# Performance work log

Hardware: AMD Instinct MI355X
Metric: run time of the kernel (lower is better)

The kernel has to match this reference:

```python
import jax, jax.numpy as jnp
import numpy as np

L, B, N, C, H = 6, 4, 512, 512, 8
D = C // H          # head_dim = 64
MLP = 4 * C         # mlp_ratio = 4.0
EPS = 1e-6


def setup_inputs() -> dict:
    key = jax.random.key(0)
    ks = jax.random.split(key, 12)
    p = lambda k, sh: jax.random.normal(k, sh, dtype=jnp.float32) * 0.02
    return {
        "x": jax.random.normal(ks[0], (B, N, C), dtype=jnp.float32),
        "time_emb": jax.random.normal(ks[1], (B, C), dtype=jnp.float32),
        "pair_emb": jax.random.normal(ks[2], (B, H, N, N), dtype=jnp.float32) * 0.1,
        "is_padded_mask": jnp.zeros((B, 1, 1, N), dtype=bool),
        # per-block stacked params (leading dim = L blocks)
        "wq": p(ks[3], (L, C, C)),
        "wk": p(ks[4], (L, C, C)),
        "wv": p(ks[5], (L, C, C)),
        "wo": p(ks[6], (L, C, C)),
        "bo": jnp.zeros((L, C), dtype=jnp.float32),
        "w1": p(ks[7], (L, C, MLP)),
        "b1": jnp.zeros((L, MLP), dtype=jnp.float32),
        "w2": p(ks[8], (L, MLP, C)),
        "b2": jnp.zeros((L, C), dtype=jnp.float32),
        "wada": p(ks[9], (L, C, 6 * C)),
        "bada": jnp.zeros((L, 6 * C), dtype=jnp.float32),
    }


def _ln(x):
    # LayerNorm without affine, eps=1e-6 (torch elementwise_affine=False)
    mu = jnp.mean(x, axis=-1, keepdims=True)
    var = jnp.mean(jnp.square(x - mu), axis=-1, keepdims=True)
    return (x - mu) * jax.lax.rsqrt(var + EPS)


def _modulate(x, shift, scale):
    return x * (1.0 + scale[:, None, :]) + shift[:, None, :]


def reference(x, time_emb, pair_emb, is_padded_mask,
              wq, wk, wv, wo, bo, w1, b1, w2, b2, wada, bada):
    scale = D ** -0.5
    t_act = jax.nn.silu(time_emb)  # shared SiLU input to adaLN of each block
    for i in range(L):
        ada = t_act @ wada[i] + bada[i]  # (B, 6C)
        sh_msa, sc_msa, g_msa, sh_mlp, sc_mlp, g_mlp = jnp.split(ada, 6, axis=1)
        # fill_attn_mask: masked_fill padded key positions with -inf
        pair = jnp.where(is_padded_mask, -jnp.inf, pair_emb)  # (B,H,N,N)
        mx = _modulate(_ln(x), sh_msa, sc_msa)  # (B,N,C)
        q = (mx @ wq[i]).reshape(B, N, H, D)
        k = (mx @ wk[i]).reshape(B, N, H, D)
        v = (mx @ wv[i]).reshape(B, N, H, D)
        qk = jnp.einsum('bnhd,bshd->bhns', q, k) * scale  # (B,H,N,N)
        attn = jax.nn.softmax(qk + pair, axis=-1)
        o = jnp.einsum('bhns,bshd->bnhd', attn, v).reshape(B, N, C)
        o = o @ wo[i] + bo[i]
        x = x + g_msa[:, None, :] * o
        pair_emb = pair + qk  # residual on pair embedding
        h = _modulate(_ln(x), sh_mlp, sc_mlp)
        h = jax.nn.gelu(h @ w1[i] + b1[i], approximate=True) @ w2[i] + b2[i]
        x = x + g_mlp[:, None, :] * h
    return x, pair_emb
```

## Files before the change

kernel.cpp:

```cpp
#include <hip/hip_runtime.h>
#include <hip/hip_bf16.h>

#define LNUM 6
#define BB 4
#define NSEQ 512
#define CDIM 512
#define HNUM 8
#define DHEAD 64
#define MLPD 2048
#define MROWS (BB*NSEQ)

typedef __hip_bfloat16 bf16;
typedef __attribute__((ext_vector_type(4))) float f32x4;
typedef __attribute__((ext_vector_type(8))) short bf16x8;

__device__ __forceinline__ void gld_lds16(const bf16* g, bf16* l) {
  __builtin_amdgcn_global_load_lds((const __attribute__((address_space(1))) void*)g,
                                   (__attribute__((address_space(3))) void*)l, 16, 0, 0);
}

__device__ __forceinline__ short f2bs(float f) {
  bf16 h = __float2bfloat16(f);
  short s; __builtin_memcpy(&s, &h, 2); return s;
}

__device__ __forceinline__ float gelu_tanh(float t) {
  float u = 0.7978845608028654f * (t + 0.044715f * t * t * t);
  u = fminf(fmaxf(u, -15.f), 15.f);
  float e = __expf(2.f * u);
  return 0.5f * t * (1.f + (e - 1.f) / (e + 1.f));
}

enum { EP_BF16 = 0, EP_RESID = 2, EP_GELU = 3 };

template<int MODE>
__global__ __launch_bounds__(256) void gemm_nt(
    const bf16* __restrict__ A, int lda,
    const bf16* __restrict__ Bt, int ldb,
    int K, int zdiv,
    long sA1, long sA2, long sB1, long sB2, long sO1, long sO2,
    bf16* __restrict__ obf, int ldo,
    const float* __restrict__ bias,
    const float* __restrict__ ada, int gate_off,
    float* __restrict__ xres)
{
  __shared__ bf16 lA[2 * 64 * 64];
  __shared__ bf16 lB[2 * 64 * 64];
  const int tid = threadIdx.x;
  const int wid = tid >> 6, lane = tid & 63;
  const int z = blockIdx.z;
  const long z1 = z / zdiv, z2 = z % zdiv;
  A  += z1 * sA1 + z2 * sA2;
  Bt += z1 * sB1 + z2 * sB2;
  const long obase = z1 * sO1 + z2 * sO2;
  const int m0 = blockIdx.x * 64;
  const int n0 = blockIdx.y * 64;
  const int wm = wid >> 1, wn = wid & 1;
  const int srow = tid >> 3, scl = tid & 7;

  f32x4 zero = {0.f, 0.f, 0.f, 0.f};
  f32x4 acc[2][2];
#pragma unroll
  for (int i = 0; i < 2; i++)
#pragma unroll
    for (int j = 0; j < 2; j++) acc[i][j] = zero;

  auto stage = [&](int buf, int kt) {
#pragma unroll
    for (int r = 0; r < 2; r++) {
      const int rr = (r << 5) + srow;
      const int gk = (scl ^ (rr & 7)) << 3;
      gld_lds16(A + (size_t)(m0 + rr) * lda + (kt << 6) + gk,
                lA + buf * 4096 + (r << 11) + (wid << 9));
    }
#pragma unroll
    for (int r = 0; r < 2; r++) {
      const int rr = (r << 5) + srow;
      const int gk = (scl ^ (rr & 7)) << 3;
      gld_lds16(Bt + (size_t)(n0 + rr) * ldb + (kt << 6) + gk,
                lB + buf * 4096 + (r << 11) + (wid << 9));
    }
  };

  const int rlo = lane & 15, kq = lane >> 4;
  auto compute = [&](int buf) {
    bf16x8 af[2][2], bg[2][2];
#pragma unroll
    for (int kk = 0; kk < 2; kk++) {
#pragma unroll
      for (int i = 0; i < 2; i++) {
        const int ra = (wm << 5) + (i << 4) + rlo;
        af[kk][i] = *(const bf16x8*)(lA + buf * 4096 + (ra << 6) +
                                     ((((kk << 2) + kq) ^ (ra & 7)) << 3));
        const int rb2 = (wn << 5) + (i << 4) + rlo;
        bg[kk][i] = *(const bf16x8*)(lB + buf * 4096 + (rb2 << 6) +
                                     ((((kk << 2) + kq) ^ (rb2 & 7)) << 3));
      }
    }
#pragma unroll
    for (int kk = 0; kk < 2; kk++)
#pragma unroll
      for (int i = 0; i < 2; i++)
#pragma unroll
        for (int j = 0; j < 2; j++)
          acc[i][j] = __builtin_amdgcn_mfma_f32_16x16x32_bf16(af[kk][i], bg[kk][j], acc[i][j], 0, 0, 0);
  };

  const int NT = K >> 6;
  stage(0, 0);
  for (int t = 0; t < NT - 1; t++) {
    stage((t + 1) & 1, t + 1);
    asm volatile("s_waitcnt vmcnt(4)" ::: "memory");
    __builtin_amdgcn_s_barrier();
    asm volatile("" ::: "memory");
    compute(t & 1);
    asm volatile("" ::: "memory");
    __builtin_amdgcn_s_barrier();
  }
  asm volatile("s_waitcnt vmcnt(0)" ::: "memory");
  __builtin_amdgcn_s_barrier();
  asm volatile("" ::: "memory");
  compute((NT - 1) & 1);

  const int cl = lane & 15, rb = (lane >> 4) << 2;
#pragma unroll
  for (int i = 0; i < 2; i++) {
#pragma unroll
    for (int j = 0; j < 2; j++) {
      const int gc = n0 + (wn << 5) + (j << 4) + cl;
#pragma unroll
      for (int r = 0; r < 4; r++) {
        const int gr = m0 + (wm << 5) + (i << 4) + rb + r;
        float v = acc[i][j][r];
        if (MODE == EP_BF16) {
          obf[obase + (size_t)gr * ldo + gc] = __float2bfloat16(v);
        } else if (MODE == EP_RESID) {
          const int b = gr >> 9;
          float t2 = v + bias[gc];
          xres[(size_t)gr * CDIM + gc] += ada[b * (6 * CDIM) + gate_off + gc] * t2;
        } else {
          float t2 = v + bias[gc];
          obf[obase + (size_t)gr * ldo + gc] = __float2bfloat16(gelu_tanh(t2));
        }
      }
    }
  }
}

__global__ __launch_bounds__(256) void attn_fused(
    const bf16* __restrict__ qkv, const bf16* __restrict__ vt,
    const float* __restrict__ pair_in, float* __restrict__ pair_out,
    const unsigned char* __restrict__ mask,
    bf16* __restrict__ obuf, float scale)
{
  __shared__ bf16 lQ[64 * 64];
  __shared__ bf16 lK[2][64 * 64];
  __shared__ bf16 lV[2][64 * 64];
  __shared__ bf16 lP[64 * 64];
  const int tid = threadIdx.x, wid = tid >> 6, lane = tid & 63;
  const int z = blockIdx.z, b = z >> 3, h = z & 7;
  const int m0 = blockIdx.x * 64;
  const int srow = tid >> 3, scl = tid & 7;
  const bf16* Aq = qkv + (size_t)b * NSEQ * 1536 + h * 64;
  const bf16* Bk = Aq + CDIM;
  const bf16* Bv = vt + (size_t)z * DHEAD * NSEQ;
  const size_t pz = (size_t)z * NSEQ * NSEQ;

#pragma unroll
  for (int r = 0; r < 2; r++) {
    const int rr = (r << 5) + srow;
    const int gk = (scl ^ (rr & 7)) << 3;
    gld_lds16(Aq + (size_t)(m0 + rr) * 1536 + gk, lQ + (r << 11) + (wid << 9));
    gld_lds16(Bk + (size_t)rr * 1536 + gk, lK[0] + (r << 11) + (wid << 9));
    gld_lds16(Bv + (size_t)rr * NSEQ + gk, lV[0] + (r << 11) + (wid << 9));
  }

  const int rlo = lane & 15, kq = lane >> 4, cl = rlo;
  float m_run[4], l_run[4];
  f32x4 oacc[4];
  f32x4 zero = {0.f, 0.f, 0.f, 0.f};
#pragma unroll
  for (int r = 0; r < 4; r++) { m_run[r] = -INFINITY; l_run[r] = 0.f; }
#pragma unroll
  for (int j = 0; j < 4; j++) oacc[j] = zero;
  bf16x8 afq[2];

  for (int ct = 0; ct < 8; ct++) {
    const int cur = ct & 1;
    asm volatile("s_waitcnt vmcnt(0)" ::: "memory");
    __builtin_amdgcn_s_barrier();
    asm volatile("" ::: "memory");

    if (ct < 7) {
#pragma unroll
      for (int r = 0; r < 2; r++) {
        const int rr = (r << 5) + srow;
        const int gk = (scl ^ (rr & 7)) << 3;
        gld_lds16(Bk + (size_t)((ct + 1) * 64 + rr) * 1536 + gk,
                  lK[cur ^ 1] + (r << 11) + (wid << 9));
        gld_lds16(Bv + (size_t)rr * NSEQ + (ct + 1) * 64 + gk,
                  lV[cur ^ 1] + (r << 11) + (wid << 9));
      }
    }

    if (ct == 0) {
#pragma unroll
      for (int kk = 0; kk < 2; kk++) {
        const int ra = (wid << 4) + rlo;
        afq[kk] = *(const bf16x8*)(lQ + (ra << 6) + ((((kk << 1) << 1) + kq) == 0 ? 0 : 0));
      }
#pragma unroll
      for (int kk = 0; kk < 2; kk++) {
        const int ra = (wid << 4) + rlo;
        afq[kk] = *(const bf16x8*)(lQ + (ra << 6) + ((((kk << 2) + kq) ^ (ra & 7)) << 3));
      }
    }

    float pr[4][4];
#pragma unroll
    for (int j = 0; j < 4; j++)
#pragma unroll
      for (int r = 0; r < 4; r++)
        pr[j][r] = pair_in[pz + (size_t)(m0 + (wid << 4) + (kq << 2) + r) * NSEQ +
                           (ct * 64 + (j << 4) + cl)];
    bool mk[4];
#pragma unroll
    for (int j = 0; j < 4; j++)
      mk[j] = mask[b * NSEQ + ct * 64 + (j << 4) + cl] != 0;

    f32x4 s[4];
#pragma unroll
    for (int j = 0; j < 4; j++) s[j] = zero;
#pragma unroll
    for (int kk = 0; kk < 2; kk++)
#pragma unroll
      for (int j = 0; j < 4; j++) {
        const int rk = (j << 4) + rlo;
        bf16x8 bk = *(const bf16x8*)(lK[cur] + (rk << 6) + ((((kk << 2) + kq) ^ (rk & 7)) << 3));
        s[j] = __builtin_amdgcn_mfma_f32_16x16x32_bf16(afq[kk], bk, s[j], 0, 0, 0);
      }

    float p[4][4];
#pragma unroll
    for (int r = 0; r < 4; r++) {
      const size_t prow = pz + (size_t)(m0 + (wid << 4) + (kq << 2) + r) * NSEQ + ct * 64;
      float sf[4];
#pragma unroll
      for (int j = 0; j < 4; j++) {
        float pp = mk[j] ? -INFINITY : pr[j][r];
        sf[j] = s[j][r] * scale + pp;
        pair_out[prow + (j << 4) + cl] = sf[j];
      }
      float tm = fmaxf(fmaxf(sf[0], sf[1]), fmaxf(sf[2], sf[3]));
#pragma unroll
      for (int o = 1; o < 16; o <<= 1) tm = fmaxf(tm, __shfl_xor(tm, o));
      const float mnew = fmaxf(m_run[r], tm);
      const float fr = __expf(m_run[r] - mnew);
      float rs = 0.f;
#pragma unroll
      for (int j = 0; j < 4; j++) { p[j][r] = __expf(sf[j] - mnew); rs += p[j][r]; }
#pragma unroll
      for (int o = 1; o < 16; o <<= 1) rs += __shfl_xor(rs, o);
      l_run[r] = l_run[r] * fr + rs;
      m_run[r] = mnew;
#pragma unroll
      for (int j = 0; j < 4; j++) oacc[j][r] *= fr;
    }

#pragma unroll
    for (int j = 0; j < 4; j++)
#pragma unroll
      for (int r = 0; r < 4; r++) {
        const int row = (wid << 4) + (kq << 2) + r;
        const int col = (j << 4) + cl;
        lP[(row << 6) + (((col >> 3) ^ (row & 7)) << 3) + (col & 7)] = __float2bfloat16(p[j][r]);
      }
    asm volatile("s_waitcnt lgkmcnt(0)" ::: "memory");
    __builtin_amdgcn_sched_barrier(0);

#pragma unroll
    for (int kk = 0; kk < 2; kk++) {
      const int ra = (wid << 4) + rlo;
      bf16x8 ap = *(const bf16x8*)(lP + (ra << 6) + ((((kk << 2) + kq) ^ (ra & 7)) << 3));
#pragma unroll
      for (int j = 0; j < 4; j++) {
        const int rd = (j << 4) + rlo;
        bf16x8 bv = *(const bf16x8*)(lV[cur] + (rd << 6) + ((((kk << 2) + kq) ^ (rd & 7)) << 3));
        oacc[j] = __builtin_amdgcn_mfma_f32_16x16x32_bf16(ap, bv, oacc[j], 0, 0, 0);
      }
    }
  }

#pragma unroll
  for (int j = 0; j < 4; j++)
#pragma unroll
    for (int r = 0; r < 4; r++) {
      const int gr = m0 + (wid << 4) + (kq << 2) + r;
      const int gc = h * 64 + (j << 4) + cl;
      obuf[((size_t)b * NSEQ + gr) * CDIM + gc] = __float2bfloat16(oacc[j][r] / l_run[r]);
    }
}

__global__ __launch_bounds__(256) void ln_mod(const float* __restrict__ x,
                                              const float* __restrict__ ada,
                                              int sh_off, int sc_off,
                                              bf16* __restrict__ out)
{
  const int row = blockIdx.x;
  const int b = row >> 9;
  const float* xr = x + (size_t)row * CDIM;
  const int t = threadIdx.x;
  float2 v = ((const float2*)xr)[t];
  float s = v.x + v.y;
  float ss = v.x * v.x + v.y * v.y;
#pragma unroll
  for (int o = 32; o > 0; o >>= 1) { s += __shfl_down(s, o); ss += __shfl_down(ss, o); }
  __shared__ float red[8];
  __shared__ float mv[2];
  const int w = t >> 6, ln = t & 63;
  if (ln == 0) { red[w] = s; red[4 + w] = ss; }
  __syncthreads();
  if (t == 0) {
    float S = red[0] + red[1] + red[2] + red[3];
    float SS = red[4] + red[5] + red[6] + red[7];
    float mu = S * (1.0f / CDIM);
    float var = SS * (1.0f / CDIM) - mu * mu;
    mv[0] = mu; mv[1] = rsqrtf(var + 1e-6f);
  }
  __syncthreads();
  const float mu = mv[0], rs = mv[1];
  const float* adab = ada + b * (6 * CDIM);
  const int c = t * 2;
  float o0 = (v.x - mu) * rs * (1.0f + adab[sc_off + c])     + adab[sh_off + c];
  float o1 = (v.y - mu) * rs * (1.0f + adab[sc_off + c + 1]) + adab[sh_off + c + 1];
  out[(size_t)row * CDIM + c]     = __float2bfloat16(o0);
  out[(size_t)row * CDIM + c + 1] = __float2bfloat16(o1);
}

__global__ __launch_bounds__(256) void ada_part(const float* __restrict__ te,
                                                const float* __restrict__ wada,
                                                float* __restrict__ partial)
{
  __shared__ float ta[4][64];
  const int layer = blockIdx.z, kc = blockIdx.y;
  const int t = threadIdx.x;
  {
    const int b = t >> 6, kk = t & 63;
    float xx = te[b * CDIM + kc * 64 + kk];
    ta[b][kk] = xx / (1.f + __expf(-xx));
  }
  __syncthreads();
  const int col = blockIdx.x * 512 + t * 2;
  const float* W = wada + ((size_t)layer * CDIM + kc * 64) * 3072 + col;
  float2 acc0 = {0, 0}, acc1 = {0, 0}, acc2 = {0, 0}, acc3 = {0, 0};
#pragma unroll 8
  for (int kk = 0; kk < 64; kk++) {
    float2 w = *(const float2*)(W + (size_t)kk * 3072);
    acc0.x = fmaf(ta[0][kk], w.x, acc0.x); acc0.y = fmaf(ta[0][kk], w.y, acc0.y);
    acc1.x = fmaf(ta[1][kk], w.x, acc1.x); acc1.y = fmaf(ta[1][kk], w.y, acc1.y);
    acc2.x = fmaf(ta[2][kk], w.x, acc2.x); acc2.y = fmaf(ta[2][kk], w.y, acc2.y);
    acc3.x = fmaf(ta[3][kk], w.x, acc3.x); acc3.y = fmaf(ta[3][kk], w.y, acc3.y);
  }
  float* pp = partial + (((size_t)(layer * 8 + kc) * 4) * 3072);
  *(float2*)(pp + 0 * 3072 + col) = acc0;
  *(float2*)(pp + 1 * 3072 + col) = acc1;
  *(float2*)(pp + 2 * 3072 + col) = acc2;
  *(float2*)(pp + 3 * 3072 + col) = acc3;
}

__global__ __launch_bounds__(256) void ada_reduce(const float* __restrict__ partial,
                                                  const float* __restrict__ bada,
                                                  float* __restrict__ adab)
{
  const int idx = blockIdx.x * 256 + threadIdx.x;
  const int layer = idx / 12288, rem = idx % 12288;
  const int b = rem / 3072, col = rem % 3072;
  float acc = bada[layer * 3072 + col];
#pragma unroll
  for (int kc = 0; kc < 8; kc++)
    acc += partial[((size_t)(layer * 8 + kc) * 4 + b) * 3072 + col];
  adab[((size_t)layer * 4 + b) * 3072 + col] = acc;
}

__global__ __launch_bounds__(256) void conv_t(const float* __restrict__ src, bf16* __restrict__ dst,
                                              int R, int Ccols, long sS, long sD)
{
  src += (size_t)blockIdx.z * sS;
  dst += (size_t)blockIdx.z * sD;
  __shared__ float tb[32][33];
  const int c0 = blockIdx.x * 32, r0 = blockIdx.y * 32;
  const int tx = threadIdx.x & 31, ty = threadIdx.x >> 5;
#pragma unroll
  for (int i = ty; i < 32; i += 8) tb[i][tx] = src[(size_t)(r0 + i) * Ccols + c0 + tx];
  __syncthreads();
#pragma unroll
  for (int i = ty; i < 32; i += 8) dst[(size_t)(c0 + i) * R + r0 + tx] = __float2bfloat16(tb[tx][i]);
}

__global__ __launch_bounds__(256) void vtrans(const bf16* __restrict__ qkv, bf16* __restrict__ vt)
{
  const int z = blockIdx.z, b = z >> 3, h = z & 7;
  const bf16* src = qkv + (size_t)b * NSEQ * 1536 + 2 * CDIM + h * DHEAD;
  bf16* dst = vt + (size_t)z * DHEAD * NSEQ;
  __shared__ bf16 tb[32][33];
  const int n0 = blockIdx.x * 32, d0 = blockIdx.y * 32;
  const int tx = threadIdx.x & 31, ty = threadIdx.x >> 5;
#pragma unroll
  for (int i = ty; i < 32; i += 8) tb[i][tx] = src[(size_t)(n0 + i) * 1536 + d0 + tx];
  __syncthreads();
#pragma unroll
  for (int i = ty; i < 32; i += 8) dst[(size_t)(d0 + i) * NSEQ + n0 + tx] = tb[tx][i];
}

extern "C" void kernel_launch(void* const* d_in, const int* in_sizes, int n_in,
                              void* d_out, int out_size, void* d_ws, size_t ws_size,
                              hipStream_t stream)
{
  (void)in_sizes; (void)n_in; (void)out_size; (void)ws_size;
  const float* in_x    = (const float*)d_in[0];
  const float* in_te   = (const float*)d_in[1];
  const float* in_pair = (const float*)d_in[2];
  const unsigned char* in_mask = (const unsigned char*)d_in[3];
  const float* wq   = (const float*)d_in[4];
  const float* wk   = (const float*)d_in[5];
  const float* wv   = (const float*)d_in[6];
  const float* wo   = (const float*)d_in[7];
  const float* bo   = (const float*)d_in[8];
  const float* w1   = (const float*)d_in[9];
  const float* b1   = (const float*)d_in[10];
  const float* w2   = (const float*)d_in[11];
  const float* b2   = (const float*)d_in[12];
  const float* wada = (const float*)d_in[13];
  const float* bada = (const float*)d_in[14];

  float* xout = (float*)d_out;
  float* pairout = xout + (size_t)BB * NSEQ * CDIM;

  char* ws = (char*)d_ws;
  size_t off = 0;
  auto alloc = [&](size_t bytes) -> void* {
    void* p = ws + off; off += (bytes + 255) & ~(size_t)255; return p;
  };
  bf16*  wqkvT = (bf16*)alloc((size_t)LNUM * 1536 * 512 * 2);
  bf16*  woT   = (bf16*)alloc((size_t)LNUM * 512 * 512 * 2);
  bf16*  w1T   = (bf16*)alloc((size_t)LNUM * 2048 * 512 * 2);
  bf16*  w2T   = (bf16*)alloc((size_t)LNUM * 512 * 2048 * 2);
  float* adab  = (float*)alloc((size_t)LNUM * BB * 6 * CDIM * 4);
  float* apart = (float*)alloc((size_t)LNUM * 8 * BB * 3072 * 4);
  bf16*  mx    = (bf16*)alloc((size_t)MROWS * CDIM * 2);
  bf16*  qkv   = (bf16*)alloc((size_t)MROWS * 1536 * 2);
  bf16*  vt    = (bf16*)alloc((size_t)BB * HNUM * DHEAD * NSEQ * 2);
  bf16*  obuf  = (bf16*)alloc((size_t)MROWS * CDIM * 2);
  bf16*  hbuf  = (bf16*)alloc((size_t)MROWS * MLPD * 2);

  hipMemcpyAsync(xout, in_x, (size_t)MROWS * CDIM * 4, hipMemcpyDeviceToDevice, stream);

  conv_t<<<dim3(16, 16, LNUM), 256, 0, stream>>>(wq, wqkvT,               512, 512,  (long)512 * 512,  (long)1536 * 512);
  conv_t<<<dim3(16, 16, LNUM), 256, 0, stream>>>(wk, wqkvT + 512 * 512,   512, 512,  (long)512 * 512,  (long)1536 * 512);
  conv_t<<<dim3(16, 16, LNUM), 256, 0, stream>>>(wv, wqkvT + 2 * 512 * 512, 512, 512, (long)512 * 512, (long)1536 * 512);
  conv_t<<<dim3(16, 16, LNUM), 256, 0, stream>>>(wo, woT,                 512, 512,  (long)512 * 512,  (long)512 * 512);
  conv_t<<<dim3(64, 16, LNUM), 256, 0, stream>>>(w1, w1T,                 512, 2048, (long)512 * 2048, (long)2048 * 512);
  conv_t<<<dim3(16, 64, LNUM), 256, 0, stream>>>(w2, w2T,                 2048, 512, (long)2048 * 512, (long)512 * 2048);

  ada_part<<<dim3(6, 8, LNUM), 256, 0, stream>>>(in_te, wada, apart);
  ada_reduce<<<dim3(LNUM * BB * 3072 / 256), 256, 0, stream>>>(apart, bada, adab);

  const float scale = 0.125f;
  for (int i = 0; i < LNUM; i++) {
    const float* adal = adab + (size_t)i * BB * 6 * CDIM;
    ln_mod<<<MROWS, 256, 0, stream>>>(xout, adal, 0, CDIM, mx);
    gemm_nt<EP_BF16><<<dim3(32, 24, 1), 256, 0, stream>>>(
        mx, CDIM, wqkvT + (size_t)i * 1536 * 512, CDIM, CDIM, 1,
        0, 0, 0, 0, 0, 0,
        qkv, 1536, nullptr, nullptr, 0, nullptr);
    vtrans<<<dim3(16, 2, 32), 256, 0, stream>>>(qkv, vt);
    const float* pin = (i == 0) ? in_pair : pairout;
    attn_fused<<<dim3(8, 1, 32), 256, 0, stream>>>(qkv, vt, pin, pairout, in_mask, obuf, scale);
    gemm_nt<EP_RESID><<<dim3(32, 8, 1), 256, 0, stream>>>(
        obuf, CDIM, woT + (size_t)i * CDIM * CDIM, CDIM, CDIM, 1,
        0, 0, 0, 0, 0, 0,
        nullptr, CDIM, bo + (size_t)i * CDIM, adal, 2 * CDIM, xout);
    ln_mod<<<MROWS, 256, 0, stream>>>(xout, adal, 3 * CDIM, 4 * CDIM, mx);
    gemm_nt<EP_GELU><<<dim3(32, 32, 1), 256, 0, stream>>>(
        mx, CDIM, w1T + (size_t)i * MLPD * CDIM, CDIM, CDIM, 1,
        0, 0, 0, 0, 0, 0,
        hbuf, MLPD, b1 + (size_t)i * MLPD, nullptr, 0, nullptr);
    gemm_nt<EP_RESID><<<dim3(32, 8, 1), 256, 0, stream>>>(
        hbuf, MLPD, w2T + (size_t)i * CDIM * MLPD, MLPD, MLPD, 1,
        0, 0, 0, 0, 0, 0,
        nullptr, CDIM, b2 + (size_t)i * CDIM, adal, 5 * CDIM, xout);
  }
}
```

Before: 542.5 us.

## Template GEMM tiles, fuse V transpose into QKV epilogue, prefetch pair tiles

Templates the GEMM on tile shape and launches QKV with 128x64 tiles and the MLP up-projection with 128x128 tiles, giving fewer blocks and more reuse per block. The QKV epilogue writes V directly in transposed per-head layout, which removes the separate vtrans kernel and its extra pass over V. The attention kernel loads the next tile's pair_emb and mask values into registers during the current iteration to hide global-load latency. In exchange there are scattered, uncoalesced stores for V, higher register pressure, and fewer blocks for the larger-tile launches.

```diff
diff --git a/kernel.cpp b/kernel.cpp
--- a/kernel.cpp
+++ b/kernel.cpp
@@ -19,11 +19,6 @@
                                    (__attribute__((address_space(3))) void*)l, 16, 0, 0);
 }
 
-__device__ __forceinline__ short f2bs(float f) {
-  bf16 h = __float2bfloat16(f);
-  short s; __builtin_memcpy(&s, &h, 2); return s;
-}
-
 __device__ __forceinline__ float gelu_tanh(float t) {
   float u = 0.7978845608028654f * (t + 0.044715f * t * t * t);
   u = fminf(fmaxf(u, -15.f), 15.f);
@@ -31,9 +26,9 @@
   return 0.5f * t * (1.f + (e - 1.f) / (e + 1.f));
 }
 
-enum { EP_BF16 = 0, EP_RESID = 2, EP_GELU = 3 };
-
-template<int MODE>
+enum { EP_BF16 = 0, EP_RESID = 2, EP_GELU = 3, EP_QKV = 4 };
+
+template<int BM, int BN, int MODE>
 __global__ __launch_bounds__(256) void gemm_nt(
     const bf16* __restrict__ A, int lda,
     const bf16* __restrict__ Bt, int ldb,
@@ -42,10 +37,12 @@
     bf16* __restrict__ obf, int ldo,
     const float* __restrict__ bias,
     const float* __restrict__ ada, int gate_off,
-    float* __restrict__ xres)
-{
-  __shared__ bf16 lA[2 * 64 * 64];
-  __shared__ bf16 lB[2 * 64 * 64];
+    float* __restrict__ xres,
+    bf16* __restrict__ vtout)
+{
+  constexpr int FM = BM / 32, FN = BN / 32;
+  __shared__ bf16 lA[2 * BM * 64];
+  __shared__ bf16 lB[2 * BN * 64];
   const int tid = threadIdx.x;
   const int wid = tid >> 6, lane = tid & 63;
   const int z = blockIdx.z;
@@ -53,64 +50,67 @@
   A  += z1 * sA1 + z2 * sA2;
   Bt += z1 * sB1 + z2 * sB2;
   const long obase = z1 * sO1 + z2 * sO2;
-  const int m0 = blockIdx.x * 64;
-  const int n0 = blockIdx.y * 64;
+  const int m0 = blockIdx.x * BM;
+  const int n0 = blockIdx.y * BN;
   const int wm = wid >> 1, wn = wid & 1;
   const int srow = tid >> 3, scl = tid & 7;
 
   f32x4 zero = {0.f, 0.f, 0.f, 0.f};
-  f32x4 acc[2][2];
-#pragma unroll
-  for (int i = 0; i < 2; i++)
-#pragma unroll
-    for (int j = 0; j < 2; j++) acc[i][j] = zero;
+  f32x4 acc[FM][FN];
+#pragma unroll
+  for (int i = 0; i < FM; i++)
+#pragma unroll
+    for (int j = 0; j < FN; j++) acc[i][j] = zero;
 
   auto stage = [&](int buf, int kt) {
 #pragma unroll
-    for (int r = 0; r < 2; r++) {
-      const int rr = (r << 5) + srow;
+    for (int p = 0; p < BM / 32; p++) {
+      const int rr = (p << 5) + srow;
       const int gk = (scl ^ (rr & 7)) << 3;
       gld_lds16(A + (size_t)(m0 + rr) * lda + (kt << 6) + gk,
-                lA + buf * 4096 + (r << 11) + (wid << 9));
-    }
-#pragma unroll
-    for (int r = 0; r < 2; r++) {
-      const int rr = (r << 5) + srow;
+                lA + buf * (BM * 64) + (p << 11) + (wid << 9));
+    }
+#pragma unroll
+    for (int p = 0; p < BN / 32; p++) {
+      const int rr = (p << 5) + srow;
       const int gk = (scl ^ (rr & 7)) << 3;
       gld_lds16(Bt + (size_t)(n0 + rr) * ldb + (kt << 6) + gk,
-                lB + buf * 4096 + (r << 11) + (wid << 9));
+                lB + buf * (BN * 64) + (p << 11) + (wid << 9));
     }
   };
 
   const int rlo = lane & 15, kq = lane >> 4;
   auto compute = [&](int buf) {
-    bf16x8 af[2][2], bg[2][2];
 #pragma unroll
     for (int kk = 0; kk < 2; kk++) {
-#pragma unroll
-      for (int i = 0; i < 2; i++) {
-        const int ra = (wm << 5) + (i << 4) + rlo;
-        af[kk][i] = *(const bf16x8*)(lA + buf * 4096 + (ra << 6) +
-                                     ((((kk << 2) + kq) ^ (ra & 7)) << 3));
-        const int rb2 = (wn << 5) + (i << 4) + rlo;
-        bg[kk][i] = *(const bf16x8*)(lB + buf * 4096 + (rb2 << 6) +
-                                     ((((kk << 2) + kq) ^ (rb2 & 7)) << 3));
-      }
-    }
-#pragma unroll
-    for (int kk = 0; kk < 2; kk++)
-#pragma unroll
-      for (int i = 0; i < 2; i++)
-#pragma unroll
-        for (int j = 0; j < 2; j++)
-          acc[i][j] = __builtin_amdgcn_mfma_f32_16x16x32_bf16(af[kk][i], bg[kk][j], acc[i][j], 0, 0, 0);
+      bf16x8 af[FM], bg[FN];
+#pragma unroll
+      for (int i = 0; i < FM; i++) {
+        const int ra = wm * (BM / 2) + (i << 4) + rlo;
+        af[i] = *(const bf16x8*)(lA + buf * (BM * 64) + (ra << 6) +
+                                 ((((kk << 2) + kq) ^ (ra & 7)) << 3));
+      }
+#pragma unroll
+      for (int j = 0; j < FN; j++) {
+        const int rb2 = wn * (BN / 2) + (j << 4) + rlo;
+        bg[j] = *(const bf16x8*)(lB + buf * (BN * 64) + (rb2 << 6) +
+                                 ((((kk << 2) + kq) ^ (rb2 & 7)) << 3));
+      }
+#pragma unroll
+      for (int i = 0; i < FM; i++)
+#pragma unroll
+        for (int j = 0; j < FN; j++)
+          acc[i][j] = __builtin_amdgcn_mfma_f32_16x16x32_bf16(af[i], bg[j], acc[i][j], 0, 0, 0);
+    }
   };
 
   const int NT = K >> 6;
   stage(0, 0);
   for (int t = 0; t < NT - 1; t++) {
     stage((t + 1) & 1, t + 1);
-    asm volatile("s_waitcnt vmcnt(4)" ::: "memory");
+    if constexpr ((BM + BN) / 32 == 4)      asm volatile("s_waitcnt vmcnt(4)" ::: "memory");
+    else if constexpr ((BM + BN) / 32 == 6) asm volatile("s_waitcnt vmcnt(6)" ::: "memory");
+    else                                    asm volatile("s_waitcnt vmcnt(8)" ::: "memory");
     __builtin_amdgcn_s_barrier();
     asm volatile("" ::: "memory");
     compute(t & 1);
@@ -124,16 +124,23 @@
 
   const int cl = lane & 15, rb = (lane >> 4) << 2;
 #pragma unroll
-  for (int i = 0; i < 2; i++) {
-#pragma unroll
-    for (int j = 0; j < 2; j++) {
-      const int gc = n0 + (wn << 5) + (j << 4) + cl;
+  for (int i = 0; i < FM; i++) {
+#pragma unroll
+    for (int j = 0; j < FN; j++) {
+      const int gc = n0 + wn * (BN / 2) + (j << 4) + cl;
 #pragma unroll
       for (int r = 0; r < 4; r++) {
-        const int gr = m0 + (wm << 5) + (i << 4) + rb + r;
+        const int gr = m0 + wm * (BM / 2) + (i << 4) + rb + r;
         float v = acc[i][j][r];
         if (MODE == EP_BF16) {
           obf[obase + (size_t)gr * ldo + gc] = __float2bfloat16(v);
+        } else if (MODE == EP_QKV) {
+          if (gc < 2 * CDIM) {
+            obf[obase + (size_t)gr * ldo + gc] = __float2bfloat16(v);
+          } else {
+            const int b = gr >> 9, n = gr & 511, hd = gc - 2 * CDIM;
+            vtout[((size_t)((b << 3) + (hd >> 6)) * 64 + (hd & 63)) * 512 + n] = __float2bfloat16(v);
+          }
         } else if (MODE == EP_RESID) {
           const int b = gr >> 9;
           float t2 = v + bias[gc];
@@ -157,7 +164,8 @@
   __shared__ bf16 lK[2][64 * 64];
   __shared__ bf16 lV[2][64 * 64];
   __shared__ bf16 lP[64 * 64];
-  const int tid = threadIdx.x, wid = tid >> 6, lane = tid & 63;
+  const int tid = threadIdx.x, wid = tid >> 6;
+  const int lane = tid & 63;
   const int z = blockIdx.z, b = z >> 3, h = z & 7;
   const int m0 = blockIdx.x * 64;
   const int srow = tid >> 3, scl = tid & 7;
@@ -165,6 +173,7 @@
   const bf16* Bk = Aq + CDIM;
   const bf16* Bv = vt + (size_t)z * DHEAD * NSEQ;
   const size_t pz = (size_t)z * NSEQ * NSEQ;
+  const int rlo = lane & 15, kq = lane >> 4, cl = rlo;
 
 #pragma unroll
   for (int r = 0; r < 2; r++) {
@@ -175,7 +184,6 @@
     gld_lds16(Bv + (size_t)rr * NSEQ + gk, lV[0] + (r << 11) + (wid << 9));
   }
 
-  const int rlo = lane & 15, kq = lane >> 4, cl = rlo;
   float m_run[4], l_run[4];
   f32x4 oacc[4];
   f32x4 zero = {0.f, 0.f, 0.f, 0.f};
@@ -184,12 +192,30 @@
 #pragma unroll
   for (int j = 0; j < 4; j++) oacc[j] = zero;
   bf16x8 afq[2];
+
+  float prA[4][4]; bool mkA[4];
+  float prB[4][4]; bool mkB[4];
+#pragma unroll
+  for (int j = 0; j < 4; j++) {
+#pragma unroll
+    for (int r = 0; r < 4; r++)
+      prA[j][r] = pair_in[pz + (size_t)(m0 + (wid << 4) + (kq << 2) + r) * NSEQ + ((j << 4) + cl)];
+    mkA[j] = mask[b * NSEQ + (j << 4) + cl] != 0;
+  }
 
   for (int ct = 0; ct < 8; ct++) {
     const int cur = ct & 1;
     asm volatile("s_waitcnt vmcnt(0)" ::: "memory");
     __builtin_amdgcn_s_barrier();
     asm volatile("" ::: "memory");
+
+    if (ct == 0) {
+#pragma unroll
+      for (int kk = 0; kk < 2; kk++) {
+        const int ra = (wid << 4) + rlo;
+        afq[kk] = *(const bf16x8*)(lQ + (ra << 6) + ((((kk << 2) + kq) ^ (ra & 7)) << 3));
+      }
+    }
 
     if (ct < 7) {
 #pragma unroll
@@ -201,32 +227,15 @@
         gld_lds16(Bv + (size_t)rr * NSEQ + (ct + 1) * 64 + gk,
                   lV[cur ^ 1] + (r << 11) + (wid << 9));
       }
-    }
-
-    if (ct == 0) {
-#pragma unroll
-      for (int kk = 0; kk < 2; kk++) {
-        const int ra = (wid << 4) + rlo;
-        afq[kk] = *(const bf16x8*)(lQ + (ra << 6) + ((((kk << 1) << 1) + kq) == 0 ? 0 : 0));
-      }
-#pragma unroll
-      for (int kk = 0; kk < 2; kk++) {
-        const int ra = (wid << 4) + rlo;
-        afq[kk] = *(const bf16x8*)(lQ + (ra << 6) + ((((kk << 2) + kq) ^ (ra & 7)) << 3));
-      }
-    }
-
-    float pr[4][4];
-#pragma unroll
-    for (int j = 0; j < 4; j++)
-#pragma unroll
-      for (int r = 0; r < 4; r++)
-        pr[j][r] = pair_in[pz + (size_t)(m0 + (wid << 4) + (kq << 2) + r) * NSEQ +
-                           (ct * 64 + (j << 4) + cl)];
-    bool mk[4];
-#pragma unroll
-    for (int j = 0; j < 4; j++)
-      mk[j] = mask[b * NSEQ + ct * 64 + (j << 4) + cl] != 0;
+#pragma unroll
+      for (int j = 0; j < 4; j++) {
+#pragma unroll
+        for (int r = 0; r < 4; r++)
+          prB[j][r] = pair_in[pz + (size_t)(m0 + (wid << 4) + (kq << 2) + r) * NSEQ +
+                              ((ct + 1) * 64 + (j << 4) + cl)];
+        mkB[j] = mask[b * NSEQ + (ct + 1) * 64 + (j << 4) + cl] != 0;
+      }
+    }
 
     f32x4 s[4];
 #pragma unroll
@@ -247,7 +256,7 @@
       float sf[4];
 #pragma unroll
       for (int j = 0; j < 4; j++) {
-        float pp = mk[j] ? -INFINITY : pr[j][r];
+        float pp = mkA[j] ? -INFINITY : prA[j][r];
         sf[j] = s[j][r] * scale + pp;
         pair_out[prow + (j << 4) + cl] = sf[j];
       }
@@ -287,6 +296,15 @@
         const int rd = (j << 4) + rlo;
         bf16x8 bv = *(const bf16x8*)(lV[cur] + (rd << 6) + ((((kk << 2) + kq) ^ (rd & 7)) << 3));
         oacc[j] = __builtin_amdgcn_mfma_f32_16x16x32_bf16(ap, bv, oacc[j], 0, 0, 0);
+      }
+    }
+
+    if (ct < 7) {
+#pragma unroll
+      for (int j = 0; j < 4; j++) {
+#pragma unroll
+        for (int r = 0; r < 4; r++) prA[j][r] = prB[j][r];
+        mkA[j] = mkB[j];
       }
     }
   }
@@ -395,21 +413,6 @@
   __syncthreads();
 #pragma unroll
   for (int i = ty; i < 32; i += 8) dst[(size_t)(c0 + i) * R + r0 + tx] = __float2bfloat16(tb[tx][i]);
-}
-
-__global__ __launch_bounds__(256) void vtrans(const bf16* __restrict__ qkv, bf16* __restrict__ vt)
-{
-  const int z = blockIdx.z, b = z >> 3, h = z & 7;
-  const bf16* src = qkv + (size_t)b * NSEQ * 1536 + 2 * CDIM + h * DHEAD;
-  bf16* dst = vt + (size_t)z * DHEAD * NSEQ;
-  __shared__ bf16 tb[32][33];
-  const int n0 = blockIdx.x * 32, d0 = blockIdx.y * 32;
-  const int tx = threadIdx.x & 31, ty = threadIdx.x >> 5;
-#pragma unroll
-  for (int i = ty; i < 32; i += 8) tb[i][tx] = src[(size_t)(n0 + i) * 1536 + d0 + tx];
-  __syncthreads();
-#pragma unroll
-  for (int i = ty; i < 32; i += 8) dst[(size_t)(d0 + i) * NSEQ + n0 + tx] = tb[tx][i];
 }
 
 extern "C" void kernel_launch(void* const* d_in, const int* in_sizes, int n_in,
@@ -469,25 +472,24 @@
   for (int i = 0; i < LNUM; i++) {
     const float* adal = adab + (size_t)i * BB * 6 * CDIM;
     ln_mod<<<MROWS, 256, 0, stream>>>(xout, adal, 0, CDIM, mx);
-    gemm_nt<EP_BF16><<<dim3(32, 24, 1), 256, 0, stream>>>(
+    gemm_nt<128, 64, EP_QKV><<<dim3(16, 24, 1), 256, 0, stream>>>(
         mx, CDIM, wqkvT + (size_t)i * 1536 * 512, CDIM, CDIM, 1,
         0, 0, 0, 0, 0, 0,
-        qkv, 1536, nullptr, nullptr, 0, nullptr);
-    vtrans<<<dim3(16, 2, 32), 256, 0, stream>>>(qkv, vt);
+        qkv, 1536, nullptr, nullptr, 0, nullptr, vt);
     const float* pin = (i == 0) ? in_pair : pairout;
     attn_fused<<<dim3(8, 1, 32), 256, 0, stream>>>(qkv, vt, pin, pairout, in_mask, obuf, scale);
-    gemm_nt<EP_RESID><<<dim3(32, 8, 1), 256, 0, stream>>>(
+    gemm_nt<64, 64, EP_RESID><<<dim3(32, 8, 1), 256, 0, stream>>>(
         obuf, CDIM, woT + (size_t)i * CDIM * CDIM, CDIM, CDIM, 1,
         0, 0, 0, 0, 0, 0,
-        nullptr, CDIM, bo + (size_t)i * CDIM, adal, 2 * CDIM, xout);
+        nullptr, CDIM, bo + (size_t)i * CDIM, adal, 2 * CDIM, xout, nullptr);
     ln_mod<<<MROWS, 256, 0, stream>>>(xout, adal, 3 * CDIM, 4 * CDIM, mx);
-    gemm_nt<EP_GELU><<<dim3(32, 32, 1), 256, 0, stream>>>(
+    gemm_nt<128, 128, EP_GELU><<<dim3(16, 16, 1), 256, 0, stream>>>(
         mx, CDIM, w1T + (size_t)i * MLPD * CDIM, CDIM, CDIM, 1,
         0, 0, 0, 0, 0, 0,
-        hbuf, MLPD, b1 + (size_t)i * MLPD, nullptr, 0, nullptr);
-    gemm_nt<EP_RESID><<<dim3(32, 8, 1), 256, 0, stream>>>(
+        hbuf, MLPD, b1 + (size_t)i * MLPD, nullptr, 0, nullptr, nullptr);
+    gemm_nt<64, 64, EP_RESID><<<dim3(32, 8, 1), 256, 0, stream>>>(
         hbuf, MLPD, w2T + (size_t)i * CDIM * MLPD, MLPD, MLPD, 1,
         0, 0, 0, 0, 0, 0,
-        nullptr, CDIM, b2 + (size_t)i * CDIM, adal, 5 * CDIM, xout);
-  }
-}
+        nullptr, CDIM, b2 + (size_t)i * CDIM, adal, 5 * CDIM, xout, nullptr);
+  }
+}
```

Measured after the change: 592.1 us. 9.1% more time.
